# Performance work log

Measured on AMD Instinct MI355X. Metric: run time of the kernel, lower is better.

Reference implementation:

```python
import jax, jax.numpy as jnp
import numpy as np

B, T, C = 2, 2048, 1024
H = 16
HS = C // H  # 64
LN_EPS = 1e-5

def setup_inputs() -> dict:
    key = jax.random.key(0)
    ks = jax.random.split(key, 12)
    s = lambda *sh: 0.02
    inp = {
        'x': jax.random.normal(ks[0], (B, T, C), jnp.float32),
        # per-head Q/K/V weights (bias=False), stacked over heads: [H, C, HS]
        'wq': jax.random.normal(ks[1], (H, C, HS), jnp.float32) * 0.02,
        'wk': jax.random.normal(ks[2], (H, C, HS), jnp.float32) * 0.02,
        'wv': jax.random.normal(ks[3], (H, C, HS), jnp.float32) * 0.02,
        'w_proj': jax.random.normal(ks[4], (C, C), jnp.float32) * 0.02,
        'b_proj': jnp.zeros((C,), jnp.float32),
        'w1': jax.random.normal(ks[5], (C, 4 * C), jnp.float32) * 0.02,
        'b1': jnp.zeros((4 * C,), jnp.float32),
        'w2': jax.random.normal(ks[6], (4 * C, C), jnp.float32) * 0.02,
        'b2': jnp.zeros((C,), jnp.float32),
        'ln1_g': jnp.ones((C,), jnp.float32),
        'ln1_b': jnp.zeros((C,), jnp.float32),
        'ln2_g': jnp.ones((C,), jnp.float32),
        'ln2_b': jnp.zeros((C,), jnp.float32),
    }
    return inp

def _layernorm(x, g, b):
    mu = jnp.mean(x, axis=-1, keepdims=True)
    var = jnp.mean(jnp.square(x - mu), axis=-1, keepdims=True)
    return (x - mu) * jax.lax.rsqrt(var + LN_EPS) * g + b

def reference(x, wq, wk, wv, w_proj, b_proj, w1, b1, w2, b2, ln1_g, ln1_b, ln2_g, ln2_b):
    Bx, Tx, Cx = x.shape
    h = _layernorm(x, ln1_g, ln1_b)
    q = jnp.einsum('btc,hcd->bhtd', h, wq)
    k = jnp.einsum('btc,hcd->bhtd', h, wk)
    v = jnp.einsum('btc,hcd->bhtd', h, wv)
    # NOTE: original scales by n_embedding**-0.5 (C), not head_size**-0.5
    scores = jnp.einsum('bhtd,bhsd->bhts', q, k) * (Cx ** -0.5)
    causal = jnp.tril(jnp.ones((Tx, Tx), bool))
    scores = jnp.where(causal, scores, -jnp.inf)
    att = jax.nn.softmax(scores, axis=-1)  # [B,H,T,T]
    out = jnp.einsum('bhts,bhsd->bhtd', att, v)
    out = out.transpose(0, 2, 1, 3).reshape(Bx, Tx, Cx)  # concat heads
    out = out @ w_proj + b_proj
    x = x + out
    h2 = _layernorm(x, ln2_g, ln2_b)
    ff = jax.nn.relu(h2 @ w1 + b1) @ w2 + b2
    return x + ff
```

## Files before the change

kernel.cpp:

```cpp
#include <hip/hip_runtime.h>
#include <hip/hip_bf16.h>
#include <stdint.h>

typedef __bf16 bf16_t;
typedef __bf16 bf16x8 __attribute__((ext_vector_type(8)));
typedef __bf16 bf16x4 __attribute__((ext_vector_type(4)));
typedef float f32x4 __attribute__((ext_vector_type(4)));

static constexpr int TT = 2048, CC = 1024;

__device__ __forceinline__ void gld_lds16(const void* g, void* l) {
  __builtin_amdgcn_global_load_lds((const __attribute__((address_space(1))) void*)g,
                                   (__attribute__((address_space(3))) void*)l, 16, 0, 0);
}

__global__ __launch_bounds__(256) void transpose_cvt(const float* __restrict__ in,
                                                     bf16_t* __restrict__ out,
                                                     int K, int N) {
  __shared__ float t[32][33];
  const int k0 = blockIdx.x * 32, n0 = blockIdx.y * 32;
  const size_t boff = (size_t)blockIdx.z * K * N;
  in += boff;
  out += boff;
  const int tx = threadIdx.x & 31, ty = threadIdx.x >> 5;
#pragma unroll
  for (int j = 0; j < 4; ++j)
    t[ty + j * 8][tx] = in[(size_t)(k0 + ty + j * 8) * N + n0 + tx];
  __syncthreads();
#pragma unroll
  for (int j = 0; j < 4; ++j)
    out[(size_t)(n0 + ty + j * 8) * K + k0 + tx] = (bf16_t)t[tx][ty + j * 8];
}

__global__ __launch_bounds__(256) void ln_f32_bf16(const float* __restrict__ x,
                                                   const float* __restrict__ g,
                                                   const float* __restrict__ b,
                                                   bf16_t* __restrict__ out) {
  const int row = blockIdx.x;
  const int tid = threadIdx.x;
  const float4 v = ((const float4*)(x + (size_t)row * CC))[tid];
  float s = v.x + v.y + v.z + v.w;
  float q = v.x * v.x + v.y * v.y + v.z * v.z + v.w * v.w;
#pragma unroll
  for (int off = 1; off < 64; off <<= 1) {
    s += __shfl_xor(s, off);
    q += __shfl_xor(q, off);
  }
  __shared__ float red[8];
  const int wave = tid >> 6, lane = tid & 63;
  if (lane == 0) { red[wave] = s; red[4 + wave] = q; }
  __syncthreads();
  s = red[0] + red[1] + red[2] + red[3];
  q = red[4] + red[5] + red[6] + red[7];
  const float mu = s * (1.0f / CC);
  float var = q * (1.0f / CC) - mu * mu;
  var = fmaxf(var, 0.f);
  const float rstd = rsqrtf(var + 1e-5f);
  const float4 gv = ((const float4*)g)[tid];
  const float4 bv = ((const float4*)b)[tid];
  bf16x4 o;
  o[0] = (bf16_t)((v.x - mu) * rstd * gv.x + bv.x);
  o[1] = (bf16_t)((v.y - mu) * rstd * gv.y + bv.y);
  o[2] = (bf16_t)((v.z - mu) * rstd * gv.z + bv.z);
  o[3] = (bf16_t)((v.w - mu) * rstd * gv.w + bv.w);
  *(bf16x4*)(out + (size_t)row * CC + tid * 4) = o;
}

template <int EPI, int BN, int DEPTH>
__global__ __launch_bounds__(256) void gemm_bt(const bf16_t* __restrict__ A,
                                               const bf16_t* __restrict__ Bt,
                                               void* __restrict__ Cout,
                                               const float* __restrict__ bias,
                                               const float* __restrict__ res,
                                               bf16_t* __restrict__ vt,
                                               int M, int N, int K) {
  constexpr int WN = BN / 2;
  constexpr int NF = BN / 32;
  constexpr int NB = BN / 32;
  __shared__ alignas(16) bf16_t As[DEPTH][128 * 64];
  __shared__ alignas(16) bf16_t Bs[DEPTH][BN * 64];
  const int tid = threadIdx.x;
  const int wave = tid >> 6, lane = tid & 63;
  const int lr = lane & 15, lg = lane >> 4;
  const int wm = wave >> 1, wn = wave & 1;

  const int gx = gridDim.x;
  const int nwg = gx * gridDim.y;
  const int orig = (int)blockIdx.y * gx + (int)blockIdx.x;
  const int wgid = (orig & 7) * (nwg >> 3) + (orig >> 3);
  const int tm0 = (wgid / gx) * 128, tn0 = (wgid % gx) * BN;

  const int sr = lane >> 3;
  const int scs = (lane & 7) ^ sr;
  const bf16_t* Ag[4];
#pragma unroll
  for (int i = 0; i < 4; ++i)
    Ag[i] = A + (size_t)(tm0 + i * 32 + wave * 8 + sr) * K + scs * 8;
  const bf16_t* Bg[NB];
#pragma unroll
  for (int i = 0; i < NB; ++i)
    Bg[i] = Bt + (size_t)(tn0 + i * 32 + wave * 8 + sr) * K + scs * 8;

  auto STAGE = [&](int k0, int buf) {
#pragma unroll
    for (int i = 0; i < 4; ++i)
      gld_lds16(Ag[i] + k0, &As[buf][(i * 32 + wave * 8) * 64]);
#pragma unroll
    for (int i = 0; i < NB; ++i)
      gld_lds16(Bg[i] + k0, &Bs[buf][(i * 32 + wave * 8) * 64]);
  };

  f32x4 acc[4][NF] = {};
  const int NT = K >> 6;

  STAGE(0, 0);
  if (DEPTH == 3 && NT > 1) {
    STAGE(64, 1);
    asm volatile("s_waitcnt vmcnt(%0)" ::"i"(4 + NB) : "memory");
  } else {
    asm volatile("s_waitcnt vmcnt(0)" ::: "memory");
  }
  __builtin_amdgcn_s_barrier();

  for (int t = 0; t < NT; ++t) {
    const int cur = t % DEPTH;
    const bf16_t* Ac = As[cur];
    const bf16_t* Bc = Bs[cur];
    const bool more = (t + DEPTH - 1) < NT;
    if (more) STAGE((t + DEPTH - 1) << 6, (t + DEPTH - 1) % DEPTH);

    __builtin_amdgcn_s_setprio(1);
#pragma unroll
    for (int kk = 0; kk < 2; ++kk) {
      const int ch = ((kk * 4 + lg) ^ (lr & 7)) * 8;
      bf16x8 af[4], bfr[NF];
#pragma unroll
      for (int n = 0; n < NF; ++n)
        bfr[n] = *(const bf16x8*)&Bc[(wn * WN + n * 16 + lr) * 64 + ch];
#pragma unroll
      for (int m = 0; m < 4; ++m)
        af[m] = *(const bf16x8*)&Ac[(wm * 64 + m * 16 + lr) * 64 + ch];
#pragma unroll
      for (int m = 0; m < 4; ++m)
#pragma unroll
        for (int n = 0; n < NF; ++n)
          acc[m][n] =
              __builtin_amdgcn_mfma_f32_16x16x32_bf16(af[m], bfr[n], acc[m][n], 0, 0, 0);
    }
    __builtin_amdgcn_s_setprio(0);
    if (DEPTH == 3 && more) {
      asm volatile("s_waitcnt vmcnt(%0)" ::"i"(4 + NB) : "memory");
    } else {
      asm volatile("s_waitcnt vmcnt(0)" ::: "memory");
    }
    __builtin_amdgcn_sched_barrier(0);
    __builtin_amdgcn_s_barrier();
  }

#pragma unroll
  for (int m = 0; m < 4; ++m) {
#pragma unroll
    for (int i = 0; i < 4; ++i) {
      const int row = tm0 + wm * 64 + m * 16 + lg * 4 + i;
#pragma unroll
      for (int n = 0; n < NF; ++n) {
        const int col = tn0 + wn * WN + n * 16 + lr;
        float v = acc[m][n][i];
        if (EPI == 1) v = fmaxf(v + bias[col], 0.f);
        if (EPI == 2) v = v + bias[col] + res[(size_t)row * N + col];
        if (EPI == 2) {
          ((float*)Cout)[(size_t)row * N + col] = v;
        } else if (EPI == 3) {
          if (col >= 2048) {
            const int hd = col - 2048;
            const size_t vidx =
                ((size_t)((row >> 11) * 16 + (hd >> 6)) * 64 + (hd & 63)) * TT + (row & (TT - 1));
            vt[vidx] = (bf16_t)v;
          } else {
            ((bf16_t*)Cout)[(size_t)row * N + col] = (bf16_t)v;
          }
        } else {
          ((bf16_t*)Cout)[(size_t)row * N + col] = (bf16_t)v;
        }
      }
    }
  }
}

__global__ __launch_bounds__(256, 3) void attn_fwd(const bf16_t* __restrict__ qkv,
                                                   const bf16_t* __restrict__ Vt,
                                                   bf16_t* __restrict__ O) {
  const int bh = blockIdx.x;
  const int bb = bh >> 4, hh = bh & 15;
  const int qt = 31 - (int)blockIdx.y;
  const int qbase = qt * 64;
  const int tid = threadIdx.x;
  const int wave = tid >> 6, lane = tid & 63;
  const int lr = lane & 15, lg = lane >> 4;
  const bf16_t* Qp = qkv + (size_t)bb * TT * 3072 + hh * 64;
  const bf16_t* Kp = Qp + 1024;
  const bf16_t* Vh = Vt + (size_t)bh * 64 * TT;

  constexpr int KLP = 72;
  constexpr int VLP = 136;
  constexpr int PLP = 136;
  __shared__ alignas(16) bf16_t Klds[128 * KLP];
  __shared__ alignas(16) bf16_t Vlds[64 * VLP];
  __shared__ alignas(16) bf16_t PlS[4][16 * PLP];
  bf16_t* Pw = PlS[wave];

  const int ksr = wave * 32 + (lane >> 3);
  const int ksc = (lane & 7) * 8;
  const int vsr = wave * 16 + (lane >> 4);
  const int vsc = (lane & 15) * 8;

  const int qrow = qbase + wave * 16;
  bf16x8 qf0, qf1;
  {
    const bf16x8 a = *(const bf16x8*)(Qp + (size_t)(qrow + lr) * 3072 + lg * 8);
    const bf16x8 b = *(const bf16x8*)(Qp + (size_t)(qrow + lr) * 3072 + 32 + lg * 8);
#pragma unroll
    for (int j = 0; j < 8; ++j) {
      qf0[j] = (bf16_t)((float)a[j] * 0.03125f);
      qf1[j] = (bf16_t)((float)b[j] * 0.03125f);
    }
  }

  f32x4 oacc[4] = {};
  float m_r[4], l_r[4];
#pragma unroll
  for (int i = 0; i < 4; ++i) { m_r[i] = -1e38f; l_r[i] = 0.f; }

  bf16x8 kpre[4], vpre[4];
#pragma unroll
  for (int i = 0; i < 4; ++i) {
    kpre[i] = *(const bf16x8*)(Kp + (size_t)(ksr + i * 8) * 3072 + ksc);
    vpre[i] = *(const bf16x8*)(Vh + (size_t)(vsr + i * 4) * TT + vsc);
  }
#pragma unroll
  for (int i = 0; i < 4; ++i) {
    *(bf16x8*)&Klds[(ksr + i * 8) * KLP + ksc] = kpre[i];
    *(bf16x8*)&Vlds[(vsr + i * 4) * VLP + vsc] = vpre[i];
  }
  __syncthreads();

  const int nt = (qt >> 1) + 1;
  for (int t = 0; t < nt; ++t) {
    const int s0 = t * 128;
    const int sn = (t + 1 < nt) ? s0 + 128 : s0;
#pragma unroll
    for (int i = 0; i < 4; ++i) {
      kpre[i] = *(const bf16x8*)(Kp + (size_t)(sn + ksr + i * 8) * 3072 + ksc);
      vpre[i] = *(const bf16x8*)(Vh + (size_t)(vsr + i * 4) * TT + sn + vsc);
    }

    const int u = (qrow - s0) >> 4;
    const int cmc = min(u | 1, 7);

    float P[8][4];
    __builtin_amdgcn_s_setprio(1);
#pragma unroll
    for (int ct = 0; ct < 8; ++ct) {
      if (ct <= cmc) {
        const bf16x8 kf0 = *(const bf16x8*)&Klds[(ct * 16 + lr) * KLP + lg * 8];
        const bf16x8 kf1 = *(const bf16x8*)&Klds[(ct * 16 + lr) * KLP + 32 + lg * 8];
        f32x4 z = {};
        z = __builtin_amdgcn_mfma_f32_16x16x32_bf16(qf0, kf0, z, 0, 0, 0);
        z = __builtin_amdgcn_mfma_f32_16x16x32_bf16(qf1, kf1, z, 0, 0, 0);
        if (ct >= u) {
          const int sg = s0 + ct * 16 + lr;
#pragma unroll
          for (int i = 0; i < 4; ++i)
            P[ct][i] = (sg > qrow + lg * 4 + i) ? -1e30f : z[i];
        } else {
#pragma unroll
          for (int i = 0; i < 4; ++i) P[ct][i] = z[i];
        }
      } else {
#pragma unroll
        for (int i = 0; i < 4; ++i) P[ct][i] = -1e30f;
      }
    }
    __builtin_amdgcn_s_setprio(0);

    float lmax[4];
#pragma unroll
    for (int i = 0; i < 4; ++i) {
      float m0 = fmaxf(fmaxf(P[0][i], P[1][i]), fmaxf(P[2][i], P[3][i]));
      float m1 = fmaxf(fmaxf(P[4][i], P[5][i]), fmaxf(P[6][i], P[7][i]));
      lmax[i] = fmaxf(m0, m1);
    }
    const bool ok = (lmax[0] <= m_r[0] + 8.f) && (lmax[1] <= m_r[1] + 8.f) &&
                    (lmax[2] <= m_r[2] + 8.f) && (lmax[3] <= m_r[3] + 8.f);
    if (!__all(ok)) {
      float rm[4] = {lmax[0], lmax[1], lmax[2], lmax[3]};
#pragma unroll
      for (int off = 1; off < 16; off <<= 1)
#pragma unroll
        for (int i = 0; i < 4; ++i) rm[i] = fmaxf(rm[i], __shfl_xor(rm[i], off));
#pragma unroll
      for (int i = 0; i < 4; ++i) {
        const float mn = fmaxf(m_r[i], rm[i]);
        const float alpha = __expf(m_r[i] - mn);
        m_r[i] = mn;
        l_r[i] *= alpha;
#pragma unroll
        for (int db = 0; db < 4; ++db) oacc[db][i] *= alpha;
      }
    }

#pragma unroll
    for (int i = 0; i < 4; ++i) {
      float ls = 0.f;
#pragma unroll
      for (int ct = 0; ct < 8; ++ct) {
        const float p = __expf(P[ct][i] - m_r[i]);
        P[ct][i] = p;
        ls += p;
      }
      l_r[i] += ls;
    }

#pragma unroll
    for (int ct = 0; ct < 8; ++ct) {
      if (ct <= cmc) {
#pragma unroll
        for (int i = 0; i < 4; ++i) {
          const int q = lg * 4 + i;
          const int col = (ct * 16 + lr) ^ ((lg >> 1) << 4);
          Pw[q * PLP + col] = (bf16_t)P[ct][i];
        }
      }
    }
    asm volatile("s_waitcnt lgkmcnt(0)" ::: "memory");
    __builtin_amdgcn_sched_barrier(0);

    const int kcm = cmc >> 1;
    __builtin_amdgcn_s_setprio(1);
#pragma unroll
    for (int kc = 0; kc < 4; ++kc) {
      if (kc <= kcm) {
        const bf16x8 pf =
            *(const bf16x8*)&Pw[lr * PLP + ((kc * 32 + lg * 8) ^ ((lr >> 3) << 4))];
#pragma unroll
        for (int db = 0; db < 4; ++db) {
          const bf16x8 vf = *(const bf16x8*)&Vlds[(db * 16 + lr) * VLP + kc * 32 + lg * 8];
          oacc[db] = __builtin_amdgcn_mfma_f32_16x16x32_bf16(pf, vf, oacc[db], 0, 0, 0);
        }
      }
    }
    __builtin_amdgcn_s_setprio(0);

    if (t + 1 < nt) {
      __syncthreads();
#pragma unroll
      for (int i = 0; i < 4; ++i) {
        *(bf16x8*)&Klds[(ksr + i * 8) * KLP + ksc] = kpre[i];
        *(bf16x8*)&Vlds[(vsr + i * 4) * VLP + vsc] = vpre[i];
      }
      __syncthreads();
    }
  }

#pragma unroll
  for (int off = 1; off < 16; off <<= 1)
#pragma unroll
    for (int i = 0; i < 4; ++i) l_r[i] += __shfl_xor(l_r[i], off);

  bf16_t* Op = O + ((size_t)bb * TT + qrow) * CC + hh * 64;
#pragma unroll
  for (int i = 0; i < 4; ++i) {
    const float rl = 1.0f / l_r[i];
#pragma unroll
    for (int db = 0; db < 4; ++db)
      Op[(size_t)(lg * 4 + i) * CC + db * 16 + lr] = (bf16_t)(oacc[db][i] * rl);
  }
}

extern "C" void kernel_launch(void* const* d_in, const int* in_sizes, int n_in,
                              void* d_out, int out_size, void* d_ws, size_t ws_size,
                              hipStream_t stream) {
  const float* x      = (const float*)d_in[0];
  const float* wq     = (const float*)d_in[1];
  const float* wk     = (const float*)d_in[2];
  const float* wv     = (const float*)d_in[3];
  const float* w_proj = (const float*)d_in[4];
  const float* b_proj = (const float*)d_in[5];
  const float* w1     = (const float*)d_in[6];
  const float* b1     = (const float*)d_in[7];
  const float* w2     = (const float*)d_in[8];
  const float* b2     = (const float*)d_in[9];
  const float* ln1_g  = (const float*)d_in[10];
  const float* ln1_b  = (const float*)d_in[11];
  const float* ln2_g  = (const float*)d_in[12];
  const float* ln2_b  = (const float*)d_in[13];

  char* ws = (char*)d_ws;
  const size_t MB = 1024 * 1024;
  bf16_t* h1    = (bf16_t*)(ws + 0);
  bf16_t* Bqkv  = (bf16_t*)(ws + 8 * MB);
  bf16_t* Bproj = (bf16_t*)(ws + 14 * MB);
  bf16_t* B1w   = (bf16_t*)(ws + 16 * MB);
  bf16_t* B2w   = (bf16_t*)(ws + 24 * MB);
  bf16_t* qkv   = (bf16_t*)(ws + 32 * MB);
  bf16_t* Obuf  = (bf16_t*)(ws + 56 * MB);
  float*  res1  = (float*)(ws + 64 * MB);
  bf16_t* Vt    = (bf16_t*)(ws + 64 * MB);
  bf16_t* h2    = (bf16_t*)(ws + 80 * MB);
  bf16_t* a1    = (bf16_t*)(ws + 32 * MB);
  float*  outp  = (float*)d_out;

  dim3 blk(256);
  transpose_cvt<<<dim3(32, 2, 16), blk, 0, stream>>>(wq, Bqkv, 1024, 64);
  transpose_cvt<<<dim3(32, 2, 16), blk, 0, stream>>>(wk, Bqkv + 1024 * 1024, 1024, 64);
  transpose_cvt<<<dim3(32, 2, 16), blk, 0, stream>>>(wv, Bqkv + 2 * 1024 * 1024, 1024, 64);
  transpose_cvt<<<dim3(32, 32, 1), blk, 0, stream>>>(w_proj, Bproj, 1024, 1024);
  transpose_cvt<<<dim3(32, 128, 1), blk, 0, stream>>>(w1, B1w, 1024, 4096);
  transpose_cvt<<<dim3(128, 32, 1), blk, 0, stream>>>(w2, B2w, 4096, 1024);

  ln_f32_bf16<<<dim3(4096), blk, 0, stream>>>(x, ln1_g, ln1_b, h1);
  gemm_bt<3, 128, 2><<<dim3(24, 32), blk, 0, stream>>>(h1, Bqkv, qkv, nullptr, nullptr, Vt,
                                                       4096, 3072, 1024);
  attn_fwd<<<dim3(32, 32), blk, 0, stream>>>(qkv, Vt, Obuf);
  gemm_bt<2, 64, 3><<<dim3(16, 32), blk, 0, stream>>>(Obuf, Bproj, res1, b_proj, x, nullptr,
                                                      4096, 1024, 1024);
  ln_f32_bf16<<<dim3(4096), blk, 0, stream>>>(res1, ln2_g, ln2_b, h2);
  gemm_bt<1, 128, 2><<<dim3(32, 32), blk, 0, stream>>>(h2, B1w, a1, b1, nullptr, nullptr,
                                                       4096, 4096, 1024);
  gemm_bt<2, 64, 3><<<dim3(16, 32), blk, 0, stream>>>(a1, B2w, outp, b2, res1, nullptr,
                                                      4096, 1024, 4096);
}
```

Baseline: 259.9 us.

## Add 256x256-tile 512-thread GEMM with XCD-aware remap for QKV and FFN1

Adds a new gemm256 kernel that uses 256x256 output tiles, 8 waves, double-buffered LDS with direct global-to-LDS loads, XOR swizzling, interleaved prefetch of the next K slabs between MFMA groups, and a workgroup-ID remap across XCDs. It replaces the 128-tile gemm_bt for the QKV projection (keeping the V-transpose epilogue) and for the first FFN GEMM. The intent is more data reuse per tile and better overlap of loads with matrix math. The cost is fewer workgroups (192 and 256), which may underfill the GPU's CUs, plus higher register and LDS pressure.

Result: slower. 268.1 us (+3.2%).

```diff
diff --git a/kernel.cpp b/kernel.cpp
--- a/kernel.cpp
+++ b/kernel.cpp
@@ -66,6 +66,122 @@
   *(bf16x4*)(out + (size_t)row * CC + tid * 4) = o;
 }
 
+template <int EPI>
+__global__ __launch_bounds__(512, 2) void gemm256(const bf16_t* __restrict__ A,
+                                                  const bf16_t* __restrict__ Bt,
+                                                  void* __restrict__ Cout,
+                                                  const float* __restrict__ bias,
+                                                  bf16_t* __restrict__ vt,
+                                                  int M, int N, int K) {
+  __shared__ alignas(16) bf16_t As[2][2][256 * 32];
+  __shared__ alignas(16) bf16_t Bs[2][2][256 * 32];
+  const int tid = threadIdx.x;
+  const int wid = tid >> 6, lane = tid & 63;
+  const int lr = lane & 15, lg = lane >> 4;
+  const int wr = wid >> 2, wc = wid & 3;
+
+  const int gx = gridDim.x;
+  const int nwg = gx * (int)gridDim.y;
+  const int orig = (int)blockIdx.y * gx + (int)blockIdx.x;
+  const int wgid = (orig & 7) * (nwg >> 3) + (orig >> 3);
+  const int tm0 = (wgid / gx) * 256, tn0 = (wgid % gx) * 256;
+
+  const int srow0 = wid * 16 + (lane >> 2);
+  const int schk = ((lane & 3) ^ (srow0 & 3)) * 8;
+  const bf16_t* Asrc[2];
+  const bf16_t* Bsrc[2];
+#pragma unroll
+  for (int i = 0; i < 2; ++i) {
+    Asrc[i] = A + (size_t)(tm0 + i * 128 + srow0) * K + schk;
+    Bsrc[i] = Bt + (size_t)(tn0 + i * 128 + srow0) * K + schk;
+  }
+  const int dsto = wid * 512;
+
+  auto STAGE_A = [&](int s, int kk) {
+    bf16_t* dst = &As[s & 1][kk][dsto];
+    const int off = s * 64 + kk * 32;
+    gld_lds16(Asrc[0] + off, dst);
+    gld_lds16(Asrc[1] + off, dst + 4096);
+  };
+  auto STAGE_B = [&](int s, int kk) {
+    bf16_t* dst = &Bs[s & 1][kk][dsto];
+    const int off = s * 64 + kk * 32;
+    gld_lds16(Bsrc[0] + off, dst);
+    gld_lds16(Bsrc[1] + off, dst + 4096);
+  };
+
+  f32x4 acc[8][4] = {};
+  const int NS = K >> 6;
+
+  STAGE_A(0, 0); STAGE_B(0, 0);
+  STAGE_A(0, 1); STAGE_B(0, 1);
+  if (NS > 1) { STAGE_A(1, 0); STAGE_B(1, 0); }
+  asm volatile("s_waitcnt vmcnt(4)" ::: "memory");
+  __builtin_amdgcn_s_barrier();
+
+  const int fchk = (lg ^ (lr & 3)) * 8;
+  for (int s = 0; s < NS; ++s) {
+    const int d = s & 1;
+#pragma unroll
+    for (int q = 0; q < 4; ++q) {
+      const int kk = q >> 1, mh = q & 1;
+      bf16x8 bf[4], af[4];
+      const bf16_t* Br = &Bs[d][kk][0];
+      const bf16_t* Ar = &As[d][kk][0];
+#pragma unroll
+      for (int n = 0; n < 4; ++n)
+        bf[n] = *(const bf16x8*)&Br[(wc * 64 + n * 16 + lr) * 32 + fchk];
+#pragma unroll
+      for (int m = 0; m < 4; ++m)
+        af[m] = *(const bf16x8*)&Ar[(wr * 128 + (mh * 4 + m) * 16 + lr) * 32 + fchk];
+      if (q == 0) { if (s + 1 < NS) STAGE_A(s + 1, 1); }
+      if (q == 1) { if (s + 1 < NS) STAGE_B(s + 1, 1); }
+      if (q == 2) { if (s + 2 < NS) STAGE_A(s + 2, 0); }
+      if (q == 3) { if (s + 2 < NS) STAGE_B(s + 2, 0); }
+      __builtin_amdgcn_sched_barrier(0);
+      __builtin_amdgcn_s_barrier();
+      asm volatile("s_waitcnt lgkmcnt(0)" ::: "memory");
+      __builtin_amdgcn_sched_barrier(0);
+      __builtin_amdgcn_s_setprio(1);
+#pragma unroll
+      for (int m = 0; m < 4; ++m)
+#pragma unroll
+        for (int n = 0; n < 4; ++n)
+          acc[mh * 4 + m][n] =
+              __builtin_amdgcn_mfma_f32_16x16x32_bf16(af[m], bf[n], acc[mh * 4 + m][n], 0, 0, 0);
+      __builtin_amdgcn_s_setprio(0);
+      if (q == 3) asm volatile("s_waitcnt vmcnt(4)" ::: "memory");
+      __builtin_amdgcn_s_barrier();
+    }
+  }
+
+#pragma unroll
+  for (int m = 0; m < 8; ++m) {
+#pragma unroll
+    for (int i = 0; i < 4; ++i) {
+      const int row = tm0 + wr * 128 + m * 16 + lg * 4 + i;
+#pragma unroll
+      for (int n = 0; n < 4; ++n) {
+        const int col = tn0 + wc * 64 + n * 16 + lr;
+        float v = acc[m][n][i];
+        if (EPI == 1) {
+          v = fmaxf(v + bias[col], 0.f);
+          ((bf16_t*)Cout)[(size_t)row * N + col] = (bf16_t)v;
+        } else {
+          if (col >= 2048) {
+            const int hd = col - 2048;
+            const size_t vidx =
+                ((size_t)((row >> 11) * 16 + (hd >> 6)) * 64 + (hd & 63)) * TT + (row & (TT - 1));
+            vt[vidx] = (bf16_t)v;
+          } else {
+            ((bf16_t*)Cout)[(size_t)row * N + col] = (bf16_t)v;
+          }
+        }
+      }
+    }
+  }
+}
+
 template <int EPI, int BN, int DEPTH>
 __global__ __launch_bounds__(256) void gemm_bt(const bf16_t* __restrict__ A,
                                                const bf16_t* __restrict__ Bt,
@@ -170,15 +286,6 @@
         if (EPI == 2) v = v + bias[col] + res[(size_t)row * N + col];
         if (EPI == 2) {
           ((float*)Cout)[(size_t)row * N + col] = v;
-        } else if (EPI == 3) {
-          if (col >= 2048) {
-            const int hd = col - 2048;
-            const size_t vidx =
-                ((size_t)((row >> 11) * 16 + (hd >> 6)) * 64 + (hd & 63)) * TT + (row & (TT - 1));
-            vt[vidx] = (bf16_t)v;
-          } else {
-            ((bf16_t*)Cout)[(size_t)row * N + col] = (bf16_t)v;
-          }
         } else {
           ((bf16_t*)Cout)[(size_t)row * N + col] = (bf16_t)v;
         }
@@ -410,7 +517,7 @@
   bf16_t* a1    = (bf16_t*)(ws + 32 * MB);
   float*  outp  = (float*)d_out;
 
-  dim3 blk(256);
+  dim3 blk(256), blk512(512);
   transpose_cvt<<<dim3(32, 2, 16), blk, 0, stream>>>(wq, Bqkv, 1024, 64);
   transpose_cvt<<<dim3(32, 2, 16), blk, 0, stream>>>(wk, Bqkv + 1024 * 1024, 1024, 64);
   transpose_cvt<<<dim3(32, 2, 16), blk, 0, stream>>>(wv, Bqkv + 2 * 1024 * 1024, 1024, 64);
@@ -419,14 +526,12 @@
   transpose_cvt<<<dim3(128, 32, 1), blk, 0, stream>>>(w2, B2w, 4096, 1024);
 
   ln_f32_bf16<<<dim3(4096), blk, 0, stream>>>(x, ln1_g, ln1_b, h1);
-  gemm_bt<3, 128, 2><<<dim3(24, 32), blk, 0, stream>>>(h1, Bqkv, qkv, nullptr, nullptr, Vt,
-                                                       4096, 3072, 1024);
+  gemm256<3><<<dim3(12, 16), blk512, 0, stream>>>(h1, Bqkv, qkv, nullptr, Vt, 4096, 3072, 1024);
   attn_fwd<<<dim3(32, 32), blk, 0, stream>>>(qkv, Vt, Obuf);
   gemm_bt<2, 64, 3><<<dim3(16, 32), blk, 0, stream>>>(Obuf, Bproj, res1, b_proj, x, nullptr,
                                                       4096, 1024, 1024);
   ln_f32_bf16<<<dim3(4096), blk, 0, stream>>>(res1, ln2_g, ln2_b, h2);
-  gemm_bt<1, 128, 2><<<dim3(32, 32), blk, 0, stream>>>(h2, B1w, a1, b1, nullptr, nullptr,
-                                                       4096, 4096, 1024);
+  gemm256<1><<<dim3(16, 16), blk512, 0, stream>>>(h2, B1w, a1, b1, nullptr, 4096, 4096, 1024);
   gemm_bt<2, 64, 3><<<dim3(16, 32), blk, 0, stream>>>(a1, B2w, outp, b2, res1, nullptr,
                                                       4096, 1024, 4096);
 }
```
